# Optimization experiments

Measured on AMD Instinct MI355X. Metric: run time of the kernel, lower is better.

## Reference

```python
import jax, jax.numpy as jnp
import numpy as np
from jax.scipy.special import logsumexp

S, L = 32768, 512  # seq_len, label_num


def setup_inputs() -> dict:
    key = jax.random.key(0)
    k1, k2, k3 = jax.random.split(key, 3)
    logit = jax.random.normal(k1, (S, L), dtype=jnp.float32)   # emissions [S, L]
    labels = jax.random.randint(k2, (S,), 0, L)                # gold path [S]
    T = jax.random.normal(k3, (L, L), dtype=jnp.float32)       # T[next, prev]
    return {"logit": logit, "labels": labels, "T": T}


def _crf_loss(logit, T, labels):
    # Forward algorithm: alpha_t[j] = logsumexp_i(alpha_{t-1}[i] + T[j, i]) + feat_t[j]
    alpha0 = logit[0]

    def step(alpha, feat):
        new_alpha = logsumexp(alpha[None, :] + T, axis=1) + feat  # [L]
        return new_alpha, None

    alpha_final, _ = jax.lax.scan(step, alpha0, logit[1:])
    log_Z = logsumexp(alpha_final)

    # Gold path score: feat_0[y0] + sum_{t>0} (feat_t[y_t] + T[y_t, y_{t-1}])
    emit = logit[0, labels[0]] + jnp.sum(logit[jnp.arange(1, logit.shape[0]), labels[1:]])
    trans = jnp.sum(T[labels[1:], labels[:-1]])
    gold = emit + trans
    return log_Z - gold


def reference(logit, labels, T):
    return _crf_loss(logit, T, labels)
```

## Files before the change

### kernel.cpp

```cpp
#include <hip/hip_runtime.h>
#include <stdint.h>


#define S_LEN 32768
#define L 512
#define CH 16
#define NCF 2048
#define NB  256
#define TPB 1024
#define LN448 6.104793232f
#define LN2   0.6931471806f

#define OFF_EAF  0
#define OFF_EAB  (256*1024)
#define OFF_G    (512*1024)
#define OFF_H    (OFF_G + 2048*512*2)
#define OFF_LSE  (OFF_H + 2048*512*2)
#define OFF_GOLD (OFF_LSE + 4104*4)
#define OFF_BAR  (OFF_GOLD + 1024)

typedef float v4f __attribute__((ext_vector_type(4)));

__device__ __forceinline__ float b2f(unsigned short u){
  return __uint_as_float(((unsigned)u) << 16);
}
__device__ __forceinline__ unsigned short f2b(float x){
  unsigned u = __float_as_uint(x);
  return (unsigned short)((u + 0x7fffu + ((u >> 16) & 1u)) >> 16);
}
__device__ __forceinline__ unsigned char to_fp8(float v){
  int u = __builtin_amdgcn_cvt_pk_fp8_f32(v, v, 0, false);
  return (unsigned char)(u & 0xff);
}

__device__ __forceinline__ void stg_u8(unsigned char* p, unsigned char v){
  __hip_atomic_store(p, v, __ATOMIC_RELAXED, __HIP_MEMORY_SCOPE_AGENT);
}
__device__ __forceinline__ void stg_u64(unsigned long long* p, unsigned long long v){
  __hip_atomic_store(p, v, __ATOMIC_RELAXED, __HIP_MEMORY_SCOPE_AGENT);
}
__device__ __forceinline__ void stg_f32(float* p, float v){
  __hip_atomic_store(p, v, __ATOMIC_RELAXED, __HIP_MEMORY_SCOPE_AGENT);
}

__device__ __forceinline__ void lds_sync(){
  asm volatile("s_waitcnt lgkmcnt(0)" ::: "memory");
  __builtin_amdgcn_sched_barrier(0);
  __builtin_amdgcn_s_barrier();
  __builtin_amdgcn_sched_barrier(0);
}

__device__ __forceinline__ void grid_bar(unsigned* bar, unsigned target){
  __syncthreads();
  if (threadIdx.x == 0) {
    __hip_atomic_fetch_add(bar, 1u, __ATOMIC_RELAXED, __HIP_MEMORY_SCOPE_AGENT);
    unsigned it = 0;
    while (__hip_atomic_load(bar, __ATOMIC_RELAXED, __HIP_MEMORY_SCOPE_AGENT) < target) {
      __builtin_amdgcn_s_sleep(8);
      if ((++it & 255u) == 0u)
        (void)__hip_atomic_load(bar, __ATOMIC_ACQUIRE, __HIP_MEMORY_SCOPE_AGENT);
    }
    __builtin_amdgcn_fence(__ATOMIC_ACQUIRE, "agent");
  }
  __syncthreads();
}

__device__ __forceinline__ float blockSum(float v, float* sred){
  #pragma unroll
  for (int off = 32; off >= 1; off >>= 1) v += __shfl_xor(v, off);
  int wid = threadIdx.x >> 6, lane = threadIdx.x & 63;
  if (lane == 0) sred[wid] = v;
  __syncthreads();
  if (threadIdx.x < 16) {
    float t = sred[threadIdx.x];
    t += __shfl_xor(t, 8); t += __shfl_xor(t, 4);
    t += __shfl_xor(t, 2); t += __shfl_xor(t, 1);
    if (threadIdx.x == 0) sred[16] = t;
  }
  __syncthreads();
  float r = sred[16];
  __syncthreads();
  return r;
}

__device__ __forceinline__ float waveMax(float v){
  #pragma unroll
  for (int off = 32; off >= 1; off >>= 1) v = fmaxf(v, __shfl_xor(v, off));
  return v;
}
__device__ __forceinline__ float waveSum(float v){
  #pragma unroll
  for (int off = 32; off >= 1; off >>= 1) v += __shfl_xor(v, off);
  return v;
}

extern "C" __global__ __launch_bounds__(TPB, 4)
void crf_fused(const float* __restrict__ logit,
               const int* __restrict__ labels,
               const float* __restrict__ T,
               float* __restrict__ out,
               unsigned char* __restrict__ EAf,
               unsigned char* __restrict__ EAb,
               unsigned short* __restrict__ G,
               unsigned short* __restrict__ H,
               float* __restrict__ lsebuf,
               float* __restrict__ part,
               unsigned* __restrict__ bar){
  __shared__ __align__(16) unsigned char Pl[2*8192];
  __shared__ float sPart[16][20];
  __shared__ float sredG[17];

  const int tidx = threadIdx.x;

  {
    int tid = blockIdx.x*TPB + tidx;
    int r    = tid & 7;
    int lane = (tid >> 3) & 63;
    int kt   = (tid >> 9) & 15;
    int R16  = tid >> 13;
    int j = R16*16 + (lane & 15);
    int i = kt*32 + ((lane >> 4) << 3) + r;
    stg_u8(EAf + tid, to_fp8(2.0f * __expf(T[j*L + i])));
    stg_u8(EAb + tid, to_fp8(2.0f * __expf(T[i*L + j])));
  }
  {
    float acc = 0.f;
    if (tidx < 128) {
      int t = blockIdx.x*128 + tidx;
      int yt = labels[t];
      float v = logit[(size_t)t*L + yt];
      if (t > 0) v += T[yt*L + labels[t-1]];
      acc = v;
    }
    float s = blockSum(acc, sredG);
    if (tidx == 0) stg_f32(part + blockIdx.x, s);
  }
  grid_bar(bar, NB);

  {
    const int w    = tidx >> 6;
    const int lane = tidx & 63;
    const int quad = lane >> 4;
    const int cl   = lane & 15;
    const bool fwd = (blockIdx.x < NB/2);
    const int  b   = fwd ? blockIdx.x : (blockIdx.x - NB/2);
    const int  cg  = fwd ? (b*16 + cl) : (1 + b*16 + cl);
    const int  cgc = min(cg, NCF-1);
    const bool isc0 = fwd && (cg == 0);
    const int  jrow0 = w*32 + quad*4;

    const long* EA = (const long*)(fwd ? EAf : EAb);
    long eA[2][16];
    #pragma unroll
    for (int mt = 0; mt < 2; ++mt)
      #pragma unroll
      for (int kt = 0; kt < 16; ++kt)
        eA[mt][kt] = EA[(((w*2 + mt)*16) + kt)*64 + lane];

    int pladdr[2];
    #pragma unroll
    for (int mt = 0; mt < 2; ++mt) {
      int r0 = jrow0 + mt*16;
      pladdr[mt] = (r0 >> 5)*512 + ((((r0 >> 3) & 3)*16 + cl) << 3) + (r0 & 7);
    }
    const int bbbase = lane*8;

    const int tstart = fwd ? (cgc*CH) : (cgc*CH + CH - 2);
    const int dstep  = fwd ? L : -L;
    const float* lp = logit + (size_t)tstart*L + jrow0;
    float4 pf0, pf1;

    float vr[2][4];
    if (fwd) {
      #pragma unroll
      for (int mt = 0; mt < 2; ++mt)
        #pragma unroll
        for (int r = 0; r < 4; ++r) vr[mt][r] = 1.0f;
    } else {
      const float* ip = logit + (size_t)(cgc*CH + CH - 1)*L + jrow0;
      float4 x0 = *(const float4*)ip, x1 = *(const float4*)(ip + 16);
      vr[0][0] = __expf(x0.x); vr[0][1] = __expf(x0.y);
      vr[0][2] = __expf(x0.z); vr[0][3] = __expf(x0.w);
      vr[1][0] = __expf(x1.x); vr[1][1] = __expf(x1.y);
      vr[1][2] = __expf(x1.z); vr[1][3] = __expf(x1.w);
    }
    float m = 0.0f;
    int par = 0;

    pf0 = *(const float4*)lp; pf1 = *(const float4*)(lp + 16);

    auto renorm_store = [&](int dst){
      float mx = fmaxf(fmaxf(fmaxf(vr[0][0],vr[0][1]), fmaxf(vr[0][2],vr[0][3])),
                       fmaxf(fmaxf(vr[1][0],vr[1][1]), fmaxf(vr[1][2],vr[1][3])));
      mx = fmaxf(mx, __shfl_xor(mx, 16));
      mx = fmaxf(mx, __shfl_xor(mx, 32));
      if (quad == 0) sPart[cl][w] = mx;
      lds_sync();
      const float4* sp = (const float4*)&sPart[cl][0];
      float4 a0 = sp[0], a1 = sp[1], a2 = sp[2], a3 = sp[3];
      float M = fmaxf(fmaxf(fmaxf(fmaxf(a0.x,a0.y),fmaxf(a0.z,a0.w)),
                            fmaxf(fmaxf(a1.x,a1.y),fmaxf(a1.z,a1.w))),
                      fmaxf(fmaxf(fmaxf(a2.x,a2.y),fmaxf(a2.z,a2.w)),
                            fmaxf(fmaxf(a3.x,a3.y),fmaxf(a3.z,a3.w))));
      float sc = 448.0f / M;
      #pragma unroll
      for (int mt = 0; mt < 2; ++mt) {
        int u = __builtin_amdgcn_cvt_pk_fp8_f32(vr[mt][0]*sc, vr[mt][1]*sc, 0, false);
        u     = __builtin_amdgcn_cvt_pk_fp8_f32(vr[mt][2]*sc, vr[mt][3]*sc, u, true);
        *(int*)&Pl[dst*8192 + pladdr[mt]] = u;
      }
      m += __logf(M) - LN448;
      lds_sync();
    };

    renorm_store(0);

    for (int k = 0; k < CH; ++k) {
      const bool last = (k == CH-1);
      const bool useF = fwd || !last;

      v4f acc0 = (v4f){0.f,0.f,0.f,0.f};
      v4f acc1 = (v4f){0.f,0.f,0.f,0.f};
      {
        const unsigned char* plr = &Pl[par*8192 + bbbase];
        #pragma unroll
        for (int kt = 0; kt < 16; ++kt) {
          long bb = *(const long*)(plr + kt*512);
          acc0 = __builtin_amdgcn_mfma_f32_16x16x32_fp8_fp8(eA[0][kt], bb, acc0, 0, 0, 0);
          acc1 = __builtin_amdgcn_mfma_f32_16x16x32_fp8_fp8(eA[1][kt], bb, acc1, 0, 0, 0);
        }
      }
      m -= LN2;

      if (useF) {
        float f0 = __expf(pf0.x), f1 = __expf(pf0.y);
        float f2 = __expf(pf0.z), f3 = __expf(pf0.w);
        float g0 = __expf(pf1.x), g1 = __expf(pf1.y);
        float g2 = __expf(pf1.z), g3 = __expf(pf1.w);
        vr[0][0] = acc0[0]*f0; vr[0][1] = acc0[1]*f1;
        vr[0][2] = acc0[2]*f2; vr[0][3] = acc0[3]*f3;
        vr[1][0] = acc1[0]*g0; vr[1][1] = acc1[1]*g1;
        vr[1][2] = acc1[2]*g2; vr[1][3] = acc1[3]*g3;
        if (k == 0 && isc0) {
          vr[0][0] = f0; vr[0][1] = f1; vr[0][2] = f2; vr[0][3] = f3;
          vr[1][0] = g0; vr[1][1] = g1; vr[1][2] = g2; vr[1][3] = g3;
          m = 0.0f;
        }
      } else {
        vr[0][0] = acc0[0]; vr[0][1] = acc0[1]; vr[0][2] = acc0[2]; vr[0][3] = acc0[3];
        vr[1][0] = acc1[0]; vr[1][1] = acc1[1]; vr[1][2] = acc1[2]; vr[1][3] = acc1[3];
      }

      const bool nextF = fwd ? (k+1 < CH) : (k+1 < CH-1);
      if (nextF) {
        lp += dstep;
        pf0 = *(const float4*)lp; pf1 = *(const float4*)(lp + 16);
      }

      if (last) {
        if (cg <= NCF-1) {
          unsigned short* dst = (fwd ? G : H) + (size_t)cg*L + jrow0;
          #pragma unroll
          for (int mt = 0; mt < 2; ++mt) {
            unsigned long long pv =
                 (unsigned long long)f2b(__logf(vr[mt][0]) + m)
              | ((unsigned long long)f2b(__logf(vr[mt][1]) + m) << 16)
              | ((unsigned long long)f2b(__logf(vr[mt][2]) + m) << 32)
              | ((unsigned long long)f2b(__logf(vr[mt][3]) + m) << 48);
            stg_u64((unsigned long long*)(dst + mt*16), pv);
          }
        }
      } else {
        renorm_store(par ^ 1);
        par ^= 1;
      }
    }
  }
  grid_bar(bar, 2*NB);

  if (blockIdx.x < 128) {
    const int w    = tidx >> 6;
    const int lane = tidx & 63;
    const int g    = blockIdx.x*16 + w;
    const int j8   = lane*8;
    if (g == 0) {
      const unsigned short* p = G + (size_t)(NCF-1)*L + j8;
      ushort4 a = *(const ushort4*)p, bq = *(const ushort4*)(p + 4);
      float v[8] = { b2f(a.x),b2f(a.y),b2f(a.z),b2f(a.w),
                     b2f(bq.x),b2f(bq.y),b2f(bq.z),b2f(bq.w) };
      float mx = v[0];
      #pragma unroll
      for (int r = 1; r < 8; ++r) mx = fmaxf(mx, v[r]);
      mx = waveMax(mx);
      float s = 0.f;
      #pragma unroll
      for (int r = 0; r < 8; ++r) s += __expf(v[r] - mx);
      s = waveSum(s);
      if (lane == 0) stg_f32(lsebuf + 2*NCF, mx + __logf(s));
    } else {
      const unsigned short* hp = H + (size_t)g*L + j8;
      const unsigned short* gp = G + (size_t)(g-1)*L + j8;
      ushort4 ha = *(const ushort4*)hp, hb = *(const ushort4*)(hp + 4);
      ushort4 ga = *(const ushort4*)gp, gb = *(const ushort4*)(gp + 4);
      float hv[8] = { b2f(ha.x),b2f(ha.y),b2f(ha.z),b2f(ha.w),
                      b2f(hb.x),b2f(hb.y),b2f(hb.z),b2f(hb.w) };
      float gv[8] = { b2f(ga.x),b2f(ga.y),b2f(ga.z),b2f(ga.w),
                      b2f(gb.x),b2f(gb.y),b2f(gb.z),b2f(gb.w) };
      float m1 = -3.0e38f, m2 = -3.0e38f;
      #pragma unroll
      for (int r = 0; r < 8; ++r) {
        float a = hv[r] + gv[r];
        m1 = fmaxf(m1, a); m2 = fmaxf(m2, hv[r]);
      }
      m1 = waveMax(m1); m2 = waveMax(m2);
      float s1 = 0.f, s2 = 0.f;
      #pragma unroll
      for (int r = 0; r < 8; ++r) {
        s1 += __expf(hv[r] + gv[r] - m1);
        s2 += __expf(hv[r] - m2);
      }
      s1 = waveSum(s1); s2 = waveSum(s2);
      if (lane == 0) {
        stg_f32(lsebuf + g,       m1 + __logf(s1));
        stg_f32(lsebuf + NCF + g, m2 + __logf(s2));
      }
    }
  }
  grid_bar(bar, 3*NB);

  if (blockIdx.x == 0) {
    float acc = 0.f;
    for (int c = tidx; c < NCF; c += TPB)
      if (c >= 1) acc += lsebuf[c] - lsebuf[NCF + c];
    if (tidx < NB) acc -= part[tidx];
    float s = blockSum(acc, sredG);
    if (tidx == 0) out[0] = lsebuf[2*NCF] + s;
  }
}

extern "C" void kernel_launch(void* const* d_in, const int* in_sizes, int n_in,
                              void* d_out, int out_size, void* d_ws, size_t ws_size,
                              hipStream_t stream){
  const float* logit = (const float*)d_in[0];
  const int* labels  = (const int*)d_in[1];
  const float* T     = (const float*)d_in[2];
  char* ws = (char*)d_ws;

  hipMemsetAsync(ws + OFF_BAR, 0, 64, stream);
  crf_fused<<<NB, TPB, 0, stream>>>(
      logit, labels, T, (float*)d_out,
      (unsigned char*)(ws + OFF_EAF), (unsigned char*)(ws + OFF_EAB),
      (unsigned short*)(ws + OFF_G), (unsigned short*)(ws + OFF_H),
      (float*)(ws + OFF_LSE), (float*)(ws + OFF_GOLD),
      (unsigned*)(ws + OFF_BAR));
}
```

Before: 152.0 us.

## Interleave two independent chunk streams per block and halve chunk length

Each block now processes two independent sequence chunks (A and B) and alternates between them. The renormalisation and fp8 pack of one chunk is overlapped with the MFMA matmul of the other, and one LDS barrier is shared per half-step instead of two per step. Chunk length is halved (CH 8, NCF 4096), which shortens the serial dependency chain but doubles the G/H boundary data and the work in the combine phase. The combine phase now runs on all blocks instead of the first 128.

```diff
diff --git a/kernel.cpp b/kernel.cpp
--- a/kernel.cpp
+++ b/kernel.cpp
@@ -4,8 +4,8 @@
 
 #define S_LEN 32768
 #define L 512
-#define CH 16
-#define NCF 2048
+#define CH 8
+#define NCF 4096
 #define NB  256
 #define TPB 1024
 #define LN448 6.104793232f
@@ -14,9 +14,9 @@
 #define OFF_EAF  0
 #define OFF_EAB  (256*1024)
 #define OFF_G    (512*1024)
-#define OFF_H    (OFF_G + 2048*512*2)
-#define OFF_LSE  (OFF_H + 2048*512*2)
-#define OFF_GOLD (OFF_LSE + 4104*4)
+#define OFF_H    (OFF_G + NCF*512*2)
+#define OFF_LSE  (OFF_H + NCF*512*2)
+#define OFF_GOLD (OFF_LSE + (2*NCF+8)*4)
 #define OFF_BAR  (OFF_GOLD + 1024)
 
 typedef float v4f __attribute__((ext_vector_type(4)));
@@ -107,7 +107,8 @@
                float* __restrict__ part,
                unsigned* __restrict__ bar){
   __shared__ __align__(16) unsigned char Pl[2*8192];
-  __shared__ float sPart[16][20];
+  __shared__ float sPartA[16][20];
+  __shared__ float sPartB[16][20];
   __shared__ float sredG[17];
 
   const int tidx = threadIdx.x;
@@ -144,141 +145,169 @@
     const int cl   = lane & 15;
     const bool fwd = (blockIdx.x < NB/2);
     const int  b   = fwd ? blockIdx.x : (blockIdx.x - NB/2);
-    const int  cg  = fwd ? (b*16 + cl) : (1 + b*16 + cl);
-    const int  cgc = min(cg, NCF-1);
-    const bool isc0 = fwd && (cg == 0);
+    const int  cgA = fwd ? (b*32 + cl)      : (1 + b*32 + cl);
+    const int  cgB = fwd ? (b*32 + 16 + cl) : (1 + b*32 + 16 + cl);
+    const int  cgcA = min(cgA, NCF-1);
+    const int  cgcB = min(cgB, NCF-1);
+    const bool isc0 = fwd && (cgA == 0);
     const int  jrow0 = w*32 + quad*4;
 
-    const long* EA = (const long*)(fwd ? EAf : EAb);
+    const long* EAp = (const long*)(fwd ? EAf : EAb);
     long eA[2][16];
     #pragma unroll
     for (int mt = 0; mt < 2; ++mt)
       #pragma unroll
       for (int kt = 0; kt < 16; ++kt)
-        eA[mt][kt] = EA[(((w*2 + mt)*16) + kt)*64 + lane];
-
-    int pladdr[2];
-    #pragma unroll
-    for (int mt = 0; mt < 2; ++mt) {
-      int r0 = jrow0 + mt*16;
-      pladdr[mt] = (r0 >> 5)*512 + ((((r0 >> 3) & 3)*16 + cl) << 3) + (r0 & 7);
+        eA[mt][kt] = EAp[(((w*2 + mt)*16) + kt)*64 + lane];
+
+    int pladdr0, pladdr1;
+    {
+      int r0 = jrow0;
+      pladdr0 = (r0 >> 5)*512 + ((((r0 >> 3) & 3)*16 + cl) << 3) + (r0 & 7);
+      r0 = jrow0 + 16;
+      pladdr1 = (r0 >> 5)*512 + ((((r0 >> 3) & 3)*16 + cl) << 3) + (r0 & 7);
     }
     const int bbbase = lane*8;
 
-    const int tstart = fwd ? (cgc*CH) : (cgc*CH + CH - 2);
-    const int dstep  = fwd ? L : -L;
-    const float* lp = logit + (size_t)tstart*L + jrow0;
-    float4 pf0, pf1;
-
-    float vr[2][4];
+    const int dstep = fwd ? L : -L;
+    const float* lpA = logit + (size_t)(fwd ? cgcA*CH : cgcA*CH + CH - 2)*L + jrow0;
+    const float* lpB = logit + (size_t)(fwd ? cgcB*CH : cgcB*CH + CH - 2)*L + jrow0;
+    float4 pA0, pA1, pB0, pB1;
+
+    v4f vA0, vA1, vB0, vB1;
     if (fwd) {
-      #pragma unroll
-      for (int mt = 0; mt < 2; ++mt)
-        #pragma unroll
-        for (int r = 0; r < 4; ++r) vr[mt][r] = 1.0f;
+      vA0 = (v4f){1.f,1.f,1.f,1.f}; vA1 = vA0; vB0 = vA0; vB1 = vA0;
     } else {
-      const float* ip = logit + (size_t)(cgc*CH + CH - 1)*L + jrow0;
+      const float* ip = logit + (size_t)(cgcA*CH + CH - 1)*L + jrow0;
       float4 x0 = *(const float4*)ip, x1 = *(const float4*)(ip + 16);
-      vr[0][0] = __expf(x0.x); vr[0][1] = __expf(x0.y);
-      vr[0][2] = __expf(x0.z); vr[0][3] = __expf(x0.w);
-      vr[1][0] = __expf(x1.x); vr[1][1] = __expf(x1.y);
-      vr[1][2] = __expf(x1.z); vr[1][3] = __expf(x1.w);
-    }
-    float m = 0.0f;
-    int par = 0;
-
-    pf0 = *(const float4*)lp; pf1 = *(const float4*)(lp + 16);
-
-    auto renorm_store = [&](int dst){
-      float mx = fmaxf(fmaxf(fmaxf(vr[0][0],vr[0][1]), fmaxf(vr[0][2],vr[0][3])),
-                       fmaxf(fmaxf(vr[1][0],vr[1][1]), fmaxf(vr[1][2],vr[1][3])));
+      vA0 = (v4f){__expf(x0.x),__expf(x0.y),__expf(x0.z),__expf(x0.w)};
+      vA1 = (v4f){__expf(x1.x),__expf(x1.y),__expf(x1.z),__expf(x1.w)};
+      ip = logit + (size_t)(cgcB*CH + CH - 1)*L + jrow0;
+      x0 = *(const float4*)ip; x1 = *(const float4*)(ip + 16);
+      vB0 = (v4f){__expf(x0.x),__expf(x0.y),__expf(x0.z),__expf(x0.w)};
+      vB1 = (v4f){__expf(x1.x),__expf(x1.y),__expf(x1.z),__expf(x1.w)};
+    }
+    float mA = 0.0f, mB = 0.0f;
+
+    pA0 = *(const float4*)lpA; pA1 = *(const float4*)(lpA + 16);
+    pB0 = *(const float4*)lpB; pB1 = *(const float4*)(lpB + 16);
+
+    auto lmax_do = [&](v4f& x0, v4f& x1, float* spw){
+      float mx = fmaxf(fmaxf(fmaxf(x0[0],x0[1]),fmaxf(x0[2],x0[3])),
+                       fmaxf(fmaxf(x1[0],x1[1]),fmaxf(x1[2],x1[3])));
       mx = fmaxf(mx, __shfl_xor(mx, 16));
       mx = fmaxf(mx, __shfl_xor(mx, 32));
-      if (quad == 0) sPart[cl][w] = mx;
+      if (quad == 0) *spw = mx;
+    };
+    auto s2_do = [&](v4f& x0, v4f& x1, const float* spbase, int plbase, float& m){
+      const float4* sp4 = (const float4*)spbase;
+      float4 q0 = sp4[0], q1 = sp4[1], q2 = sp4[2], q3 = sp4[3];
+      float M = fmaxf(fmaxf(fmaxf(fmaxf(q0.x,q0.y),fmaxf(q0.z,q0.w)),
+                            fmaxf(fmaxf(q1.x,q1.y),fmaxf(q1.z,q1.w))),
+                      fmaxf(fmaxf(fmaxf(q2.x,q2.y),fmaxf(q2.z,q2.w)),
+                            fmaxf(fmaxf(q3.x,q3.y),fmaxf(q3.z,q3.w))));
+      float sc = 448.0f / M;
+      int u0 = __builtin_amdgcn_cvt_pk_fp8_f32(x0[0]*sc, x0[1]*sc, 0, false);
+      u0     = __builtin_amdgcn_cvt_pk_fp8_f32(x0[2]*sc, x0[3]*sc, u0, true);
+      *(int*)&Pl[plbase + pladdr0] = u0;
+      int u1 = __builtin_amdgcn_cvt_pk_fp8_f32(x1[0]*sc, x1[1]*sc, 0, false);
+      u1     = __builtin_amdgcn_cvt_pk_fp8_f32(x1[2]*sc, x1[3]*sc, u1, true);
+      *(int*)&Pl[plbase + pladdr1] = u1;
+      m += __logf(M) - LN448;
+    };
+    auto mfma_do = [&](int plbase, v4f& o0, v4f& o1){
+      o0 = (v4f){0.f,0.f,0.f,0.f}; o1 = (v4f){0.f,0.f,0.f,0.f};
+      const unsigned char* plr = &Pl[plbase + bbbase];
+      #pragma unroll
+      for (int kt = 0; kt < 16; ++kt) {
+        long bb = *(const long*)(plr + kt*512);
+        o0 = __builtin_amdgcn_mfma_f32_16x16x32_fp8_fp8(eA[0][kt], bb, o0, 0, 0, 0);
+        o1 = __builtin_amdgcn_mfma_f32_16x16x32_fp8_fp8(eA[1][kt], bb, o1, 0, 0, 0);
+      }
+    };
+    auto store_out = [&](v4f& x0, v4f& x1, float m, int cg){
+      if (cg <= NCF-1) {
+        unsigned short* dst = (fwd ? G : H) + (size_t)cg*L + jrow0;
+        unsigned long long pv =
+             (unsigned long long)f2b(__logf(x0[0]) + m)
+          | ((unsigned long long)f2b(__logf(x0[1]) + m) << 16)
+          | ((unsigned long long)f2b(__logf(x0[2]) + m) << 32)
+          | ((unsigned long long)f2b(__logf(x0[3]) + m) << 48);
+        stg_u64((unsigned long long*)dst, pv);
+        pv = (unsigned long long)f2b(__logf(x1[0]) + m)
+          | ((unsigned long long)f2b(__logf(x1[1]) + m) << 16)
+          | ((unsigned long long)f2b(__logf(x1[2]) + m) << 32)
+          | ((unsigned long long)f2b(__logf(x1[3]) + m) << 48);
+        stg_u64((unsigned long long*)(dst + 16), pv);
+      }
+    };
+
+    lmax_do(vA0, vA1, &sPartA[cl][w]);
+    lmax_do(vB0, vB1, &sPartB[cl][w]);
+    lds_sync();
+    s2_do(vA0, vA1, &sPartA[cl][0], 0, mA);
+    lds_sync();
+
+    for (int k = 0; k < CH-1; ++k) {
+      {
+        v4f a0, a1;
+        mfma_do(0, a0, a1);
+        s2_do(vB0, vB1, &sPartB[cl][0], 8192, mB);
+        float f0=__expf(pA0.x), f1=__expf(pA0.y), f2=__expf(pA0.z), f3=__expf(pA0.w);
+        float g0=__expf(pA1.x), g1=__expf(pA1.y), g2=__expf(pA1.z), g3=__expf(pA1.w);
+        vA0 = (v4f){a0[0]*f0, a0[1]*f1, a0[2]*f2, a0[3]*f3};
+        vA1 = (v4f){a1[0]*g0, a1[1]*g1, a1[2]*g2, a1[3]*g3};
+        if (k == 0 && isc0) {
+          vA0 = (v4f){f0,f1,f2,f3}; vA1 = (v4f){g0,g1,g2,g3}; mA = 0.0f;
+        }
+        lpA += dstep;
+        pA0 = *(const float4*)lpA;
+        pA1 = *(const float4*)(lpA + 16);
+        lmax_do(vA0, vA1, &sPartA[cl][w]);
+        lds_sync();
+      }
+      {
+        v4f b0, b1;
+        mfma_do(8192, b0, b1);
+        s2_do(vA0, vA1, &sPartA[cl][0], 0, mA);
+        float f0=__expf(pB0.x), f1=__expf(pB0.y), f2=__expf(pB0.z), f3=__expf(pB0.w);
+        float g0=__expf(pB1.x), g1=__expf(pB1.y), g2=__expf(pB1.z), g3=__expf(pB1.w);
+        vB0 = (v4f){b0[0]*f0, b0[1]*f1, b0[2]*f2, b0[3]*f3};
+        vB1 = (v4f){b1[0]*g0, b1[1]*g1, b1[2]*g2, b1[3]*g3};
+        lpB += dstep;
+        pB0 = *(const float4*)lpB;
+        pB1 = *(const float4*)(lpB + 16);
+        lmax_do(vB0, vB1, &sPartB[cl][w]);
+        lds_sync();
+      }
+    }
+
+    {
+      v4f a0, a1;
+      mfma_do(0, a0, a1);
+      s2_do(vB0, vB1, &sPartB[cl][0], 8192, mB);
+      if (fwd) {
+        float f0=__expf(pA0.x), f1=__expf(pA0.y), f2=__expf(pA0.z), f3=__expf(pA0.w);
+        float g0=__expf(pA1.x), g1=__expf(pA1.y), g2=__expf(pA1.z), g3=__expf(pA1.w);
+        vA0 = (v4f){a0[0]*f0, a0[1]*f1, a0[2]*f2, a0[3]*f3};
+        vA1 = (v4f){a1[0]*g0, a1[1]*g1, a1[2]*g2, a1[3]*g3};
+      } else { vA0 = a0; vA1 = a1; }
+      store_out(vA0, vA1, mA - (isc0 ? (CH-1) : CH)*LN2, cgA);
       lds_sync();
-      const float4* sp = (const float4*)&sPart[cl][0];
-      float4 a0 = sp[0], a1 = sp[1], a2 = sp[2], a3 = sp[3];
-      float M = fmaxf(fmaxf(fmaxf(fmaxf(a0.x,a0.y),fmaxf(a0.z,a0.w)),
-                            fmaxf(fmaxf(a1.x,a1.y),fmaxf(a1.z,a1.w))),
-                      fmaxf(fmaxf(fmaxf(a2.x,a2.y),fmaxf(a2.z,a2.w)),
-                            fmaxf(fmaxf(a3.x,a3.y),fmaxf(a3.z,a3.w))));
-      float sc = 448.0f / M;
-      #pragma unroll
-      for (int mt = 0; mt < 2; ++mt) {
-        int u = __builtin_amdgcn_cvt_pk_fp8_f32(vr[mt][0]*sc, vr[mt][1]*sc, 0, false);
-        u     = __builtin_amdgcn_cvt_pk_fp8_f32(vr[mt][2]*sc, vr[mt][3]*sc, u, true);
-        *(int*)&Pl[dst*8192 + pladdr[mt]] = u;
-      }
-      m += __logf(M) - LN448;
-      lds_sync();
-    };
-
-    renorm_store(0);
-
-    for (int k = 0; k < CH; ++k) {
-      const bool last = (k == CH-1);
-      const bool useF = fwd || !last;
-
-      v4f acc0 = (v4f){0.f,0.f,0.f,0.f};
-      v4f acc1 = (v4f){0.f,0.f,0.f,0.f};
-      {
-        const unsigned char* plr = &Pl[par*8192 + bbbase];
-        #pragma unroll
-        for (int kt = 0; kt < 16; ++kt) {
-          long bb = *(const long*)(plr + kt*512);
-          acc0 = __builtin_amdgcn_mfma_f32_16x16x32_fp8_fp8(eA[0][kt], bb, acc0, 0, 0, 0);
-          acc1 = __builtin_amdgcn_mfma_f32_16x16x32_fp8_fp8(eA[1][kt], bb, acc1, 0, 0, 0);
-        }
-      }
-      m -= LN2;
-
-      if (useF) {
-        float f0 = __expf(pf0.x), f1 = __expf(pf0.y);
-        float f2 = __expf(pf0.z), f3 = __expf(pf0.w);
-        float g0 = __expf(pf1.x), g1 = __expf(pf1.y);
-        float g2 = __expf(pf1.z), g3 = __expf(pf1.w);
-        vr[0][0] = acc0[0]*f0; vr[0][1] = acc0[1]*f1;
-        vr[0][2] = acc0[2]*f2; vr[0][3] = acc0[3]*f3;
-        vr[1][0] = acc1[0]*g0; vr[1][1] = acc1[1]*g1;
-        vr[1][2] = acc1[2]*g2; vr[1][3] = acc1[3]*g3;
-        if (k == 0 && isc0) {
-          vr[0][0] = f0; vr[0][1] = f1; vr[0][2] = f2; vr[0][3] = f3;
-          vr[1][0] = g0; vr[1][1] = g1; vr[1][2] = g2; vr[1][3] = g3;
-          m = 0.0f;
-        }
-      } else {
-        vr[0][0] = acc0[0]; vr[0][1] = acc0[1]; vr[0][2] = acc0[2]; vr[0][3] = acc0[3];
-        vr[1][0] = acc1[0]; vr[1][1] = acc1[1]; vr[1][2] = acc1[2]; vr[1][3] = acc1[3];
-      }
-
-      const bool nextF = fwd ? (k+1 < CH) : (k+1 < CH-1);
-      if (nextF) {
-        lp += dstep;
-        pf0 = *(const float4*)lp; pf1 = *(const float4*)(lp + 16);
-      }
-
-      if (last) {
-        if (cg <= NCF-1) {
-          unsigned short* dst = (fwd ? G : H) + (size_t)cg*L + jrow0;
-          #pragma unroll
-          for (int mt = 0; mt < 2; ++mt) {
-            unsigned long long pv =
-                 (unsigned long long)f2b(__logf(vr[mt][0]) + m)
-              | ((unsigned long long)f2b(__logf(vr[mt][1]) + m) << 16)
-              | ((unsigned long long)f2b(__logf(vr[mt][2]) + m) << 32)
-              | ((unsigned long long)f2b(__logf(vr[mt][3]) + m) << 48);
-            stg_u64((unsigned long long*)(dst + mt*16), pv);
-          }
-        }
-      } else {
-        renorm_store(par ^ 1);
-        par ^= 1;
-      }
+      v4f b0, b1;
+      mfma_do(8192, b0, b1);
+      if (fwd) {
+        float f0=__expf(pB0.x), f1=__expf(pB0.y), f2=__expf(pB0.z), f3=__expf(pB0.w);
+        float g0=__expf(pB1.x), g1=__expf(pB1.y), g2=__expf(pB1.z), g3=__expf(pB1.w);
+        vB0 = (v4f){b0[0]*f0, b0[1]*f1, b0[2]*f2, b0[3]*f3};
+        vB1 = (v4f){b1[0]*g0, b1[1]*g1, b1[2]*g2, b1[3]*g3};
+      } else { vB0 = b0; vB1 = b1; }
+      store_out(vB0, vB1, mB - CH*LN2, cgB);
     }
   }
   grid_bar(bar, 2*NB);
 
-  if (blockIdx.x < 128) {
+  {
     const int w    = tidx >> 6;
     const int lane = tidx & 63;
     const int g    = blockIdx.x*16 + w;
```

After: 179.5 us. 1.18x slower.

## Prefetch emission rows into LDS via async global_load_lds triple buffering

Applied to the files above, without the earlier changes.

Emission rows for the chunked forward/backward recurrence are now staged into a triple-buffered, XOR-swizzled LDS area using global_load_lds, issued two steps ahead. The per-step barrier waits only on older vector loads (vmcnt(2)). This is meant to hide global load latency on the serial MFMA recurrence. The per-step ln2 correction is folded into one adjustment at the final store. Shared memory grows to about 115 KB of dynamic LDS per block, which limits occupancy, and the code relies on correct vmcnt accounting and swizzle indexing.

```diff
diff --git a/kernel.cpp b/kernel.cpp
--- a/kernel.cpp
+++ b/kernel.cpp
@@ -19,6 +19,12 @@
 #define OFF_GOLD (OFF_LSE + 4104*4)
 #define OFF_BAR  (OFF_GOLD + 1024)
 
+#define PL_OFF   0
+#define SP_OFF   16384
+#define SR_OFF   17664
+#define LF_OFF   18432
+#define SMEM_TOTAL (18432 + 3*32768)
+
 typedef float v4f __attribute__((ext_vector_type(4)));
 
 __device__ __forceinline__ float b2f(unsigned short u){
@@ -43,8 +49,20 @@
   __hip_atomic_store(p, v, __ATOMIC_RELAXED, __HIP_MEMORY_SCOPE_AGENT);
 }
 
+__device__ __forceinline__ void gl2lds16(const void* g, void* l){
+  __builtin_amdgcn_global_load_lds(
+      (const __attribute__((address_space(1))) void*)g,
+      (__attribute__((address_space(3))) void*)l, 16, 0, 0);
+}
+
 __device__ __forceinline__ void lds_sync(){
   asm volatile("s_waitcnt lgkmcnt(0)" ::: "memory");
+  __builtin_amdgcn_sched_barrier(0);
+  __builtin_amdgcn_s_barrier();
+  __builtin_amdgcn_sched_barrier(0);
+}
+__device__ __forceinline__ void step_sync(){
+  asm volatile("s_waitcnt vmcnt(2) lgkmcnt(0)" ::: "memory");
   __builtin_amdgcn_sched_barrier(0);
   __builtin_amdgcn_s_barrier();
   __builtin_amdgcn_sched_barrier(0);
@@ -106,9 +124,11 @@
                float* __restrict__ lsebuf,
                float* __restrict__ part,
                unsigned* __restrict__ bar){
-  __shared__ __align__(16) unsigned char Pl[2*8192];
-  __shared__ float sPart[16][20];
-  __shared__ float sredG[17];
+  extern __shared__ __align__(16) char smem[];
+  unsigned char* Pl = (unsigned char*)(smem + PL_OFF);
+  float (*sPart)[20] = (float(*)[20])(smem + SP_OFF);
+  float* sredG       = (float*)(smem + SR_OFF);
+  char*  LF          = smem + LF_OFF;
 
   const int tidx = threadIdx.x;
 
@@ -149,130 +169,161 @@
     const bool isc0 = fwd && (cg == 0);
     const int  jrow0 = w*32 + quad*4;
 
-    const long* EA = (const long*)(fwd ? EAf : EAb);
+    const int  cgw  = fwd ? (b*16 + w) : (1 + b*16 + w);
+    const int  cgcw = min(cgw, NCF-1);
+    const unsigned swzw = (unsigned)((w & 7) << 4);
+    const unsigned so   = ((unsigned)(lane*16)) ^ swzw;
+
+    const long* EAp = (const long*)(fwd ? EAf : EAb);
     long eA[2][16];
     #pragma unroll
     for (int mt = 0; mt < 2; ++mt)
       #pragma unroll
       for (int kt = 0; kt < 16; ++kt)
-        eA[mt][kt] = EA[(((w*2 + mt)*16) + kt)*64 + lane];
-
-    int pladdr[2];
-    #pragma unroll
-    for (int mt = 0; mt < 2; ++mt) {
-      int r0 = jrow0 + mt*16;
-      pladdr[mt] = (r0 >> 5)*512 + ((((r0 >> 3) & 3)*16 + cl) << 3) + (r0 & 7);
+        eA[mt][kt] = EAp[(((w*2 + mt)*16) + kt)*64 + lane];
+
+    int pladdr0, pladdr1;
+    {
+      int r0 = jrow0;
+      pladdr0 = (r0 >> 5)*512 + ((((r0 >> 3) & 3)*16 + cl) << 3) + (r0 & 7);
+      r0 = jrow0 + 16;
+      pladdr1 = (r0 >> 5)*512 + ((((r0 >> 3) & 3)*16 + cl) << 3) + (r0 & 7);
     }
     const int bbbase = lane*8;
-
-    const int tstart = fwd ? (cgc*CH) : (cgc*CH + CH - 2);
-    const int dstep  = fwd ? L : -L;
-    const float* lp = logit + (size_t)tstart*L + jrow0;
-    float4 pf0, pf1;
-
-    float vr[2][4];
+    const int scl = (cl & 7) << 4;
+    const int ib  = w*128 + quad*16;
+    const int fa0 = cl*2048 + (ib ^ scl);
+    const int fa1 = cl*2048 + ((ib + 64) ^ scl);
+
+    {
+      size_t t0 = (size_t)(fwd ? (cgcw*CH + 0) : (cgcw*CH + CH - 2 - 0));
+      size_t t1 = (size_t)(fwd ? (cgcw*CH + 1) : (cgcw*CH + CH - 2 - 1));
+      const char* r0p = (const char*)logit + t0*(L*4);
+      const char* r1p = (const char*)logit + t1*(L*4);
+      char* d0 = LF + 0*32768 + w*2048;
+      char* d1 = LF + 1*32768 + w*2048;
+      gl2lds16(r0p + so, d0);  gl2lds16(r0p + 1024 + so, d0 + 1024);
+      gl2lds16(r1p + so, d1);  gl2lds16(r1p + 1024 + so, d1 + 1024);
+    }
+
+    v4f v0, v1;
     if (fwd) {
-      #pragma unroll
-      for (int mt = 0; mt < 2; ++mt)
-        #pragma unroll
-        for (int r = 0; r < 4; ++r) vr[mt][r] = 1.0f;
+      v0 = (v4f){1.f,1.f,1.f,1.f}; v1 = v0;
     } else {
       const float* ip = logit + (size_t)(cgc*CH + CH - 1)*L + jrow0;
       float4 x0 = *(const float4*)ip, x1 = *(const float4*)(ip + 16);
-      vr[0][0] = __expf(x0.x); vr[0][1] = __expf(x0.y);
-      vr[0][2] = __expf(x0.z); vr[0][3] = __expf(x0.w);
-      vr[1][0] = __expf(x1.x); vr[1][1] = __expf(x1.y);
-      vr[1][2] = __expf(x1.z); vr[1][3] = __expf(x1.w);
+      v0 = (v4f){__expf(x0.x),__expf(x0.y),__expf(x0.z),__expf(x0.w)};
+      v1 = (v4f){__expf(x1.x),__expf(x1.y),__expf(x1.z),__expf(x1.w)};
     }
     float m = 0.0f;
     int par = 0;
-
-    pf0 = *(const float4*)lp; pf1 = *(const float4*)(lp + 16);
-
-    auto renorm_store = [&](int dst){
-      float mx = fmaxf(fmaxf(fmaxf(vr[0][0],vr[0][1]), fmaxf(vr[0][2],vr[0][3])),
-                       fmaxf(fmaxf(vr[1][0],vr[1][1]), fmaxf(vr[1][2],vr[1][3])));
+    int bo0 = 0, bo1 = 32768, bo2 = 2*32768;
+
+    {
+      float mx = fmaxf(fmaxf(fmaxf(v0[0],v0[1]),fmaxf(v0[2],v0[3])),
+                       fmaxf(fmaxf(v1[0],v1[1]),fmaxf(v1[2],v1[3])));
       mx = fmaxf(mx, __shfl_xor(mx, 16));
       mx = fmaxf(mx, __shfl_xor(mx, 32));
       if (quad == 0) sPart[cl][w] = mx;
       lds_sync();
-      const float4* sp = (const float4*)&sPart[cl][0];
-      float4 a0 = sp[0], a1 = sp[1], a2 = sp[2], a3 = sp[3];
-      float M = fmaxf(fmaxf(fmaxf(fmaxf(a0.x,a0.y),fmaxf(a0.z,a0.w)),
-                            fmaxf(fmaxf(a1.x,a1.y),fmaxf(a1.z,a1.w))),
-                      fmaxf(fmaxf(fmaxf(a2.x,a2.y),fmaxf(a2.z,a2.w)),
-                            fmaxf(fmaxf(a3.x,a3.y),fmaxf(a3.z,a3.w))));
+      const float4* sp4 = (const float4*)&sPart[cl][0];
+      float4 q0 = sp4[0], q1 = sp4[1], q2 = sp4[2], q3 = sp4[3];
+      float M = fmaxf(fmaxf(fmaxf(fmaxf(q0.x,q0.y),fmaxf(q0.z,q0.w)),
+                            fmaxf(fmaxf(q1.x,q1.y),fmaxf(q1.z,q1.w))),
+                      fmaxf(fmaxf(fmaxf(q2.x,q2.y),fmaxf(q2.z,q2.w)),
+                            fmaxf(fmaxf(q3.x,q3.y),fmaxf(q3.z,q3.w))));
       float sc = 448.0f / M;
-      #pragma unroll
-      for (int mt = 0; mt < 2; ++mt) {
-        int u = __builtin_amdgcn_cvt_pk_fp8_f32(vr[mt][0]*sc, vr[mt][1]*sc, 0, false);
-        u     = __builtin_amdgcn_cvt_pk_fp8_f32(vr[mt][2]*sc, vr[mt][3]*sc, u, true);
-        *(int*)&Pl[dst*8192 + pladdr[mt]] = u;
-      }
-      m += __logf(M) - LN448;
-      lds_sync();
-    };
-
-    renorm_store(0);
+      int u0 = __builtin_amdgcn_cvt_pk_fp8_f32(v0[0]*sc, v0[1]*sc, 0, false);
+      u0     = __builtin_amdgcn_cvt_pk_fp8_f32(v0[2]*sc, v0[3]*sc, u0, true);
+      *(int*)&Pl[pladdr0] = u0;
+      int u1 = __builtin_amdgcn_cvt_pk_fp8_f32(v1[0]*sc, v1[1]*sc, 0, false);
+      u1     = __builtin_amdgcn_cvt_pk_fp8_f32(v1[2]*sc, v1[3]*sc, u1, true);
+      *(int*)&Pl[pladdr1] = u1;
+      m = __logf(M) - LN448;
+      step_sync();
+    }
 
     for (int k = 0; k < CH; ++k) {
       const bool last = (k == CH-1);
       const bool useF = fwd || !last;
 
-      v4f acc0 = (v4f){0.f,0.f,0.f,0.f};
-      v4f acc1 = (v4f){0.f,0.f,0.f,0.f};
       {
-        const unsigned char* plr = &Pl[par*8192 + bbbase];
+        const int ks = k + 2;
+        const bool ok = fwd ? (ks <= CH-1) : (ks <= CH-2);
+        if (ok) {
+          size_t t = (size_t)(fwd ? (cgcw*CH + ks) : (cgcw*CH + CH - 2 - ks));
+          const char* row = (const char*)logit + t*(L*4);
+          char* dst = LF + bo2 + w*2048;
+          gl2lds16(row + so, dst);
+          gl2lds16(row + 1024 + so, dst + 1024);
+        }
+      }
+
+      v4f a0 = (v4f){0.f,0.f,0.f,0.f};
+      v4f a1 = (v4f){0.f,0.f,0.f,0.f};
+      {
+        const unsigned char* plr = Pl + par*8192 + bbbase;
         #pragma unroll
         for (int kt = 0; kt < 16; ++kt) {
           long bb = *(const long*)(plr + kt*512);
-          acc0 = __builtin_amdgcn_mfma_f32_16x16x32_fp8_fp8(eA[0][kt], bb, acc0, 0, 0, 0);
-          acc1 = __builtin_amdgcn_mfma_f32_16x16x32_fp8_fp8(eA[1][kt], bb, acc1, 0, 0, 0);
+          a0 = __builtin_amdgcn_mfma_f32_16x16x32_fp8_fp8(eA[0][kt], bb, a0, 0, 0, 0);
+          a1 = __builtin_amdgcn_mfma_f32_16x16x32_fp8_fp8(eA[1][kt], bb, a1, 0, 0, 0);
         }
       }
-      m -= LN2;
 
       if (useF) {
-        float f0 = __expf(pf0.x), f1 = __expf(pf0.y);
-        float f2 = __expf(pf0.z), f3 = __expf(pf0.w);
-        float g0 = __expf(pf1.x), g1 = __expf(pf1.y);
-        float g2 = __expf(pf1.z), g3 = __expf(pf1.w);
-        vr[0][0] = acc0[0]*f0; vr[0][1] = acc0[1]*f1;
-        vr[0][2] = acc0[2]*f2; vr[0][3] = acc0[3]*f3;
-        vr[1][0] = acc1[0]*g0; vr[1][1] = acc1[1]*g1;
-        vr[1][2] = acc1[2]*g2; vr[1][3] = acc1[3]*g3;
+        const char* fb = LF + bo0;
+        float4 q0 = *(const float4*)(fb + fa0);
+        float4 q1 = *(const float4*)(fb + fa1);
+        float f0=__expf(q0.x), f1=__expf(q0.y), f2=__expf(q0.z), f3=__expf(q0.w);
+        float g0=__expf(q1.x), g1=__expf(q1.y), g2=__expf(q1.z), g3=__expf(q1.w);
+        a0 = (v4f){a0[0]*f0, a0[1]*f1, a0[2]*f2, a0[3]*f3};
+        a1 = (v4f){a1[0]*g0, a1[1]*g1, a1[2]*g2, a1[3]*g3};
         if (k == 0 && isc0) {
-          vr[0][0] = f0; vr[0][1] = f1; vr[0][2] = f2; vr[0][3] = f3;
-          vr[1][0] = g0; vr[1][1] = g1; vr[1][2] = g2; vr[1][3] = g3;
-          m = 0.0f;
+          a0 = (v4f){f0,f1,f2,f3}; a1 = (v4f){g0,g1,g2,g3}; m = 0.0f;
+        }
+      }
+
+      if (last) {
+        if (cg <= NCF-1) {
+          float madj = m - (isc0 ? (float)(CH-1) : (float)CH) * LN2;
+          unsigned short* dst = (fwd ? G : H) + (size_t)cg*L + jrow0;
+          unsigned long long pv =
+               (unsigned long long)f2b(__logf(a0[0]) + madj)
+            | ((unsigned long long)f2b(__logf(a0[1]) + madj) << 16)
+            | ((unsigned long long)f2b(__logf(a0[2]) + madj) << 32)
+            | ((unsigned long long)f2b(__logf(a0[3]) + madj) << 48);
+          stg_u64((unsigned long long*)dst, pv);
+          pv = (unsigned long long)f2b(__logf(a1[0]) + madj)
+            | ((unsigned long long)f2b(__logf(a1[1]) + madj) << 16)
+            | ((unsigned long long)f2b(__logf(a1[2]) + madj) << 32)
+            | ((unsigned long long)f2b(__logf(a1[3]) + madj) << 48);
+          stg_u64((unsigned long long*)(dst + 16), pv);
         }
       } else {
-        vr[0][0] = acc0[0]; vr[0][1] = acc0[1]; vr[0][2] = acc0[2]; vr[0][3] = acc0[3];
-        vr[1][0] = acc1[0]; vr[1][1] = acc1[1]; vr[1][2] = acc1[2]; vr[1][3] = acc1[3];
-      }
-
-      const bool nextF = fwd ? (k+1 < CH) : (k+1 < CH-1);
-      if (nextF) {
-        lp += dstep;
-        pf0 = *(const float4*)lp; pf1 = *(const float4*)(lp + 16);
-      }
-
-      if (last) {
-        if (cg <= NCF-1) {
-          unsigned short* dst = (fwd ? G : H) + (size_t)cg*L + jrow0;
-          #pragma unroll
-          for (int mt = 0; mt < 2; ++mt) {
-            unsigned long long pv =
-                 (unsigned long long)f2b(__logf(vr[mt][0]) + m)
-              | ((unsigned long long)f2b(__logf(vr[mt][1]) + m) << 16)
-              | ((unsigned long long)f2b(__logf(vr[mt][2]) + m) << 32)
-              | ((unsigned long long)f2b(__logf(vr[mt][3]) + m) << 48);
-            stg_u64((unsigned long long*)(dst + mt*16), pv);
-          }
-        }
-      } else {
-        renorm_store(par ^ 1);
+        float mx = fmaxf(fmaxf(fmaxf(a0[0],a0[1]),fmaxf(a0[2],a0[3])),
+                         fmaxf(fmaxf(a1[0],a1[1]),fmaxf(a1[2],a1[3])));
+        mx = fmaxf(mx, __shfl_xor(mx, 16));
+        mx = fmaxf(mx, __shfl_xor(mx, 32));
+        if (quad == 0) sPart[cl][w] = mx;
+        lds_sync();
+        const float4* sp4 = (const float4*)&sPart[cl][0];
+        float4 q0 = sp4[0], q1 = sp4[1], q2 = sp4[2], q3 = sp4[3];
+        float M = fmaxf(fmaxf(fmaxf(fmaxf(q0.x,q0.y),fmaxf(q0.z,q0.w)),
+                              fmaxf(fmaxf(q1.x,q1.y),fmaxf(q1.z,q1.w))),
+                        fmaxf(fmaxf(fmaxf(q2.x,q2.y),fmaxf(q2.z,q2.w)),
+                              fmaxf(fmaxf(q3.x,q3.y),fmaxf(q3.z,q3.w))));
+        float sc = 448.0f / M;
+        int u0 = __builtin_amdgcn_cvt_pk_fp8_f32(a0[0]*sc, a0[1]*sc, 0, false);
+        u0     = __builtin_amdgcn_cvt_pk_fp8_f32(a0[2]*sc, a0[3]*sc, u0, true);
+        *(int*)&Pl[(par^1)*8192 + pladdr0] = u0;
+        int u1 = __builtin_amdgcn_cvt_pk_fp8_f32(a1[0]*sc, a1[1]*sc, 0, false);
+        u1     = __builtin_amdgcn_cvt_pk_fp8_f32(a1[2]*sc, a1[3]*sc, u1, true);
+        *(int*)&Pl[(par^1)*8192 + pladdr1] = u1;
+        m += __logf(M) - LN448;
+        step_sync();
         par ^= 1;
+        int tmp = bo0; bo0 = bo1; bo1 = bo2; bo2 = tmp;
       }
     }
   }
@@ -346,8 +397,15 @@
   const float* T     = (const float*)d_in[2];
   char* ws = (char*)d_ws;
 
+  static bool attr_set = false;
+  if (!attr_set) {
+    hipFuncSetAttribute((const void*)crf_fused,
+                        hipFuncAttributeMaxDynamicSharedMemorySize, SMEM_TOTAL);
+    attr_set = true;
+  }
+
   hipMemsetAsync(ws + OFF_BAR, 0, 64, stream);
-  crf_fused<<<NB, TPB, 0, stream>>>(
+  crf_fused<<<NB, TPB, SMEM_TOTAL, stream>>>(
       logit, labels, T, (float*)d_out,
       (unsigned char*)(ws + OFF_EAF), (unsigned char*)(ws + OFF_EAB),
       (unsigned short*)(ws + OFF_G), (unsigned short*)(ws + OFF_H),
```

Result: slower. 156.5 us (+2.9%).
